# Optimization experiments

Measured on AMD Instinct MI355X. Metric: run time of the kernel, lower is better.

The kernel has to match this reference:

```python
import jax, jax.numpy as jnp
import numpy as np

B, T, D = 4, 2048, 1024
DEPTH = 4
LEAF_DIM = 256
NUM_LEAVES = 2 ** DEPTH          # 16
NUM_NODES = NUM_LEAVES - 1       # 15


def _uniform(key, shape, scale):
    s = 1.0 / np.sqrt(scale)
    return jax.random.uniform(key, shape, minval=-s, maxval=s, dtype=jnp.float32)


def setup_inputs() -> dict:
    key = jax.random.key(0)
    ks = jax.random.split(key, 8)
    x = jax.random.normal(ks[0], (B, T, D), dtype=jnp.float32)
    # gate params: Dense(1) per internal node, level-order layout
    node_w = _uniform(ks[1], (NUM_NODES, D), D)
    node_b = _uniform(ks[2], (NUM_NODES,), D)
    # leaf MLP params: D -> LEAF_DIM -> D, stacked over leaves
    w1 = _uniform(ks[3], (NUM_LEAVES, D, LEAF_DIM), D)
    b1 = _uniform(ks[4], (NUM_LEAVES, LEAF_DIM), D)
    w2 = _uniform(ks[5], (NUM_LEAVES, LEAF_DIM, D), LEAF_DIM)
    b2 = _uniform(ks[6], (NUM_LEAVES, D), LEAF_DIM)
    return {"x": x, "node_w": node_w, "node_b": node_b,
            "w1": w1, "b1": b1, "w2": w2, "b2": b2, "training": 0}


def _leaf_probs(x, node_w, node_b, depth):
    # gate activations for all internal nodes at once: [B,T,NUM_NODES]
    c = jax.nn.sigmoid(jnp.einsum('btd,nd->btn', x, node_w) + node_b)
    probs = jnp.ones(c.shape[:-1] + (1,), dtype=c.dtype)
    for m in range(depth):
        start = 2 ** m - 1
        cl = c[..., start:start + 2 ** m]          # gates at level m: [B,T,2^m]
        # left child gets c, right child gets (1-c); interleave preserves
        # the recursion's n -> (2n, 2n+1) indexing
        probs = jnp.stack([probs * cl, probs * (1.0 - cl)], axis=-1)
        probs = probs.reshape(probs.shape[:-2] + (-1,))
    return probs                                   # [B,T,NUM_LEAVES]


def reference(x, node_w, node_b, w1, b1, w2, b2, training):
    num_leaves = w1.shape[0]
    depth = int(np.log2(num_leaves))
    probs = _leaf_probs(x, node_w, node_b, depth)          # [B,T,L]
    # all leaf MLP hidden layers as one batched GEMM
    h = jax.nn.relu(jnp.einsum('btd,ldh->btlh', x, w1) + b1)
    # weight hidden by leaf probability, then contract l and h together so the
    # [B,T,L,D] per-leaf output is never materialized
    h = h * probs[..., None]
    out = jnp.einsum('btlh,lhd->btd', h, w2)
    out = out + jnp.einsum('btl,ld->btd', probs, b2)
    return out
```

## Files before the change

kernel.cpp:

```cpp
#include <hip/hip_runtime.h>
#include <stdint.h>

typedef unsigned short ushort_t;
typedef __bf16 bf16x8 __attribute__((ext_vector_type(8)));
typedef float f32x4 __attribute__((ext_vector_type(4)));

#define M_TOK 8192
#define K1 1024
#define N1 4096
#define K2 4160
#define N2 1024

template <int V> struct ic { static constexpr int value = V; };

__device__ __forceinline__ ushort_t f2bf(float f) {
  union { float f; unsigned u; } v; v.f = f;
  unsigned u = v.u;
  u += 0x7FFFu + ((u >> 16) & 1u);
  return (ushort_t)(u >> 16);
}

__device__ __forceinline__ void gload16(const void* g, void* l) {
  __builtin_amdgcn_global_load_lds((__attribute__((address_space(1))) void*)g,
                                   (__attribute__((address_space(3))) void*)l,
                                   16, 0, 0);
}

__global__ __launch_bounds__(256) void k_prep(
    const float* __restrict__ x, const float* __restrict__ node_w,
    const float* __restrict__ node_b, const float* __restrict__ w1,
    const float* __restrict__ w2, const float* __restrict__ b2,
    ushort_t* __restrict__ xb, float* __restrict__ probs,
    ushort_t* __restrict__ w1t, ushort_t* __restrict__ w2t,
    ushort_t* __restrict__ hp) {
  __shared__ ushort_t tile[64][68];
  const int b = blockIdx.x;
  if (b < 1024) {
    const int tr = threadIdx.x >> 4, tc = (threadIdx.x & 15) * 4;
    const int l = b >> 6, rem = b & 63;
    const int kt = rem >> 2, ht = rem & 3;
    const float* in = w1 + (size_t)l * K1 * 256;
#pragma unroll
    for (int rr = 0; rr < 4; ++rr) {
      int r = tr + rr * 16;
      float4 v = *(const float4*)(in + (size_t)(kt * 64 + r) * 256 + ht * 64 + tc);
      tile[r][tc+0] = f2bf(v.x); tile[r][tc+1] = f2bf(v.y);
      tile[r][tc+2] = f2bf(v.z); tile[r][tc+3] = f2bf(v.w);
    }
    __syncthreads();
#pragma unroll
    for (int rr = 0; rr < 4; ++rr) {
      int oh = tr + rr * 16;
      ushort4 o;
      o.x = tile[tc+0][oh]; o.y = tile[tc+1][oh];
      o.z = tile[tc+2][oh]; o.w = tile[tc+3][oh];
      *(ushort4*)(w1t + (size_t)(l * 256 + ht * 64 + oh) * K1 + kt * 64 + tc) = o;
    }
  } else if (b < 2048) {
    const int tr = threadIdx.x >> 4, tc = (threadIdx.x & 15) * 4;
    const int bb = b - 1024;
    const int l = bb >> 6, rem = bb & 63;
    const int ht = rem >> 4, dt = rem & 15;
    const float* in = w2 + (size_t)l * 256 * N2;
#pragma unroll
    for (int rr = 0; rr < 4; ++rr) {
      int r = tr + rr * 16;
      float4 v = *(const float4*)(in + (size_t)(ht * 64 + r) * N2 + dt * 64 + tc);
      tile[r][tc+0] = f2bf(v.x); tile[r][tc+1] = f2bf(v.y);
      tile[r][tc+2] = f2bf(v.z); tile[r][tc+3] = f2bf(v.w);
    }
    __syncthreads();
#pragma unroll
    for (int rr = 0; rr < 4; ++rr) {
      int od = tr + rr * 16;
      ushort4 o;
      o.x = tile[tc+0][od]; o.y = tile[tc+1][od];
      o.z = tile[tc+2][od]; o.w = tile[tc+3][od];
      *(ushort4*)(w2t + (size_t)(dt * 64 + od) * K2 + l * 256 + ht * 64 + tc) = o;
    }
  } else if (b < 2304) {
    int tid = (b - 2048) * 256 + threadIdx.x;
    int d = tid >> 6, cc = tid & 63;
    float v = (cc < 16) ? b2[cc * N2 + d] : 0.f;
    w2t[(size_t)d * K2 + 4096 + cc] = f2bf(v);
  } else {
    const int wid = threadIdx.x >> 6, lane = threadIdx.x & 63;
    const int t = (b - 2304) * 4 + wid;
    const float* xr = x + (size_t)t * K1;
    float xv[16];
#pragma unroll
    for (int j = 0; j < 4; ++j) {
      float4 v = *(const float4*)(xr + j * 256 + lane * 4);
      xv[4*j+0] = v.x; xv[4*j+1] = v.y; xv[4*j+2] = v.z; xv[4*j+3] = v.w;
    }
    ushort_t* xbr = xb + (size_t)t * K1;
#pragma unroll
    for (int j = 0; j < 4; ++j) {
      ushort4 o;
      o.x = f2bf(xv[4*j+0]); o.y = f2bf(xv[4*j+1]);
      o.z = f2bf(xv[4*j+2]); o.w = f2bf(xv[4*j+3]);
      *(ushort4*)(xbr + j * 256 + lane * 4) = o;
    }
    float c[15];
#pragma unroll
    for (int n = 0; n < 15; ++n) {
      float s = 0.f;
      const float* wr = node_w + n * K1;
#pragma unroll
      for (int j = 0; j < 4; ++j) {
        float4 w = *(const float4*)(wr + j * 256 + lane * 4);
        s += xv[4*j+0]*w.x + xv[4*j+1]*w.y + xv[4*j+2]*w.z + xv[4*j+3]*w.w;
      }
#pragma unroll
      for (int off = 32; off > 0; off >>= 1) s += __shfl_xor(s, off);
      float z = s + node_b[n];
      c[n] = 1.f / (1.f + __expf(-z));
    }
    if (lane < 16) {
      float p = 1.f;
#pragma unroll
      for (int m = 0; m < 4; ++m) {
        int jm = lane >> (4 - m);
        int node = (1 << m) - 1 + jm;
        int bit = (lane >> (3 - m)) & 1;
        p *= bit ? (1.f - c[node]) : c[node];
      }
      probs[t * 16 + lane] = p;
      hp[(size_t)t * K2 + 4096 + lane] = f2bf(p);
    }
    if (lane < 48) hp[(size_t)t * K2 + 4112 + lane] = 0;
  }
}

template <int NT, int LDA, int LDB, int MODE>
__global__ __launch_bounds__(512, 2) void k_gemm3(
    const ushort_t* __restrict__ A, const ushort_t* __restrict__ Bt,
    const float* __restrict__ probs, const float* __restrict__ b1,
    ushort_t* __restrict__ hp, float* __restrict__ out, int ntn) {
  constexpr int ATILE = 256 * 128;
  constexpr int BTILE = 128 * 128;
  constexpr int TBYTES = ATILE + BTILE;
  extern __shared__ char lds[];
  const int tid = threadIdx.x;
  int bid = blockIdx.x;
  const int nwg = gridDim.x;
  bid = (bid & 7) * (nwg >> 3) + (bid >> 3);
  const int bm = bid / ntn, bn = bid % ntn;

  const int wid = tid >> 6, lane = tid & 63;
  const int widM = wid >> 1, widN = wid & 1;
  const int lr = lane & 15, g = lane >> 4;

  const ushort_t* Ag = A + (size_t)bm * 256 * LDA;
  const ushort_t* Bg = Bt + (size_t)bn * 128 * LDB;

  auto stageHalf = [&](char* base, int kt, int part) {
#pragma unroll
    for (int r = 0; r < 2; ++r) {
      int s = tid + part * 1024 + r * 512;
      int row = s >> 3;
      int c16 = (s & 7) ^ (row & 7);
      gload16((const char*)(Ag + (size_t)row * LDA) + kt * 128 + (c16 << 4),
              base + s * 16);
    }
    {
      int s = tid + part * 512;
      int row = s >> 3;
      int c16 = (s & 7) ^ (row & 7);
      gload16((const char*)(Bg + (size_t)row * LDB) + kt * 128 + (c16 << 4),
              base + ATILE + s * 16);
    }
  };
  auto rdA = [&](char* base, int mi, int kk) -> bf16x8 {
    int row = widM * 64 + mi * 16 + lr;
    return *(const bf16x8*)(base + row * 128 + (((kk * 4 + g) ^ (lr & 7)) << 4));
  };
  auto rdB = [&](char* base, int nj, int kk) -> bf16x8 {
    int row = widN * 64 + nj * 16 + lr;
    return *(const bf16x8*)(base + ATILE + row * 128 + (((kk * 4 + g) ^ (lr & 7)) << 4));
  };

  f32x4 acc[4][4];
#pragma unroll
  for (int i = 0; i < 4; ++i)
#pragma unroll
    for (int j = 0; j < 4; ++j) acc[i][j] = (f32x4){0.f, 0.f, 0.f, 0.f};

  bf16x8 a01[2][4];
  bf16x8 bfr[2][8];
  bf16x8 a23[4];

  char* r0 = lds;
  char* r1 = lds + TBYTES;
  char* r2 = lds + 2 * TBYTES;

  stageHalf(r0, 0, 0); stageHalf(r0, 0, 1);
  stageHalf(r1, 1, 0); stageHalf(r1, 1, 1);
  asm volatile("s_waitcnt vmcnt(6)" ::: "memory");
  __builtin_amdgcn_sched_barrier(0);
  __builtin_amdgcn_s_barrier();
  __builtin_amdgcn_sched_barrier(0);
#pragma unroll
  for (int mi = 0; mi < 2; ++mi)
#pragma unroll
    for (int kk = 0; kk < 2; ++kk) a01[0][mi * 2 + kk] = rdA(r0, mi, kk);
#pragma unroll
  for (int nj = 0; nj < 4; ++nj)
#pragma unroll
    for (int kk = 0; kk < 2; ++kk) bfr[0][nj * 2 + kk] = rdB(r0, nj, kk);

  auto body = [&](auto PARC, int kt, char* cur, char* nxt, char* stg) {
    constexpr int P = decltype(PARC)::value;
#pragma unroll
    for (int mi = 0; mi < 2; ++mi)
#pragma unroll
      for (int kk = 0; kk < 2; ++kk) a23[mi * 2 + kk] = rdA(cur, mi + 2, kk);
    if (kt + 2 < NT) stageHalf(stg, kt + 2, 0);
    __builtin_amdgcn_sched_barrier(0);
    __builtin_amdgcn_s_setprio(1);
#pragma unroll
    for (int kk = 0; kk < 2; ++kk)
#pragma unroll
      for (int nj = 0; nj < 4; ++nj)
#pragma unroll
        for (int mi = 0; mi < 2; ++mi)
          acc[mi][nj] = __builtin_amdgcn_mfma_f32_16x16x32_bf16(
              a01[P][mi * 2 + kk], bfr[P][nj * 2 + kk], acc[mi][nj], 0, 0, 0);
    __builtin_amdgcn_s_setprio(0);
    if (kt + 1 < NT) {
      if (kt + 2 < NT) asm volatile("s_waitcnt vmcnt(3)" ::: "memory");
      else             asm volatile("s_waitcnt vmcnt(0)" ::: "memory");
      __builtin_amdgcn_sched_barrier(0);
      __builtin_amdgcn_s_barrier();
      __builtin_amdgcn_sched_barrier(0);
#pragma unroll
      for (int mi = 0; mi < 2; ++mi)
#pragma unroll
        for (int kk = 0; kk < 2; ++kk) a01[P ^ 1][mi * 2 + kk] = rdA(nxt, mi, kk);
#pragma unroll
      for (int nj = 0; nj < 4; ++nj)
#pragma unroll
        for (int kk = 0; kk < 2; ++kk) bfr[P ^ 1][nj * 2 + kk] = rdB(nxt, nj, kk);
      if (kt + 2 < NT) stageHalf(stg, kt + 2, 1);
    }
    __builtin_amdgcn_sched_barrier(0);
    __builtin_amdgcn_s_setprio(1);
#pragma unroll
    for (int kk = 0; kk < 2; ++kk)
#pragma unroll
      for (int nj = 0; nj < 4; ++nj)
#pragma unroll
        for (int mi = 0; mi < 2; ++mi)
          acc[2 + mi][nj] = __builtin_amdgcn_mfma_f32_16x16x32_bf16(
              a23[mi * 2 + kk], bfr[P][nj * 2 + kk], acc[2 + mi][nj], 0, 0, 0);
    __builtin_amdgcn_s_setprio(0);
  };

  int kt = 0;
#pragma unroll 1
  for (int it = 0; it < NT / 2; ++it) {
    body(ic<0>{}, kt, r0, r1, r2); ++kt;
    { char* t = r0; r0 = r1; r1 = r2; r2 = t; }
    body(ic<1>{}, kt, r0, r1, r2); ++kt;
    { char* t = r0; r0 = r1; r1 = r2; r2 = t; }
  }
  if constexpr (NT & 1) body(ic<0>{}, kt, r0, r1, r2);

  const int rowb = bm * 256 + widM * 64 + g * 4;
  const int colb = bn * 128 + widN * 64 + lr;
  if (MODE == 0) {
    const int leaf = bn >> 1;
#pragma unroll
    for (int mi = 0; mi < 4; ++mi) {
      int rbase = rowb + mi * 16;
      float pm[4];
#pragma unroll
      for (int rg = 0; rg < 4; ++rg)
        pm[rg] = probs[(size_t)(rbase + rg) * 16 + leaf];
#pragma unroll
      for (int nj = 0; nj < 4; ++nj) {
        float bias = b1[colb + nj * 16];
#pragma unroll
        for (int rg = 0; rg < 4; ++rg) {
          float v = acc[mi][nj][rg] + bias;
          v = v > 0.f ? v : 0.f;
          v *= pm[rg];
          hp[(size_t)(rbase + rg) * K2 + colb + nj * 16] = f2bf(v);
        }
      }
    }
  } else {
#pragma unroll
    for (int mi = 0; mi < 4; ++mi) {
      int rbase = rowb + mi * 16;
#pragma unroll
      for (int nj = 0; nj < 4; ++nj)
#pragma unroll
        for (int rg = 0; rg < 4; ++rg)
          out[(size_t)(rbase + rg) * N2 + colb + nj * 16] = acc[mi][nj][rg];
    }
  }
}

extern "C" void kernel_launch(void* const* d_in, const int* in_sizes, int n_in,
                              void* d_out, int out_size, void* d_ws, size_t ws_size,
                              hipStream_t stream) {
  const float* x      = (const float*)d_in[0];
  const float* node_w = (const float*)d_in[1];
  const float* node_b = (const float*)d_in[2];
  const float* w1     = (const float*)d_in[3];
  const float* b1     = (const float*)d_in[4];
  const float* w2     = (const float*)d_in[5];
  const float* b2     = (const float*)d_in[6];
  float* out = (float*)d_out;

  char* ws = (char*)d_ws;
  ushort_t* xb    = (ushort_t*)(ws);
  ushort_t* w1t   = (ushort_t*)(ws + 16777216);
  ushort_t* w2t   = (ushort_t*)(ws + 25165824);
  ushort_t* hp    = (ushort_t*)(ws + 33685504);
  float*    probs = (float*)   (ws + 101842944);

  k_prep<<<4352, 256, 0, stream>>>(x, node_w, node_b, w1, w2, b2,
                                   xb, probs, w1t, w2t, hp);
  k_gemm3<16, K1, K1, 0><<<1024, 512, 147456, stream>>>(
      xb, w1t, probs, b1, hp, nullptr, N1 / 128);
  k_gemm3<65, K2, K2, 1><<<256, 512, 147456, stream>>>(
      hp, w2t, nullptr, nullptr, nullptr, out, N2 / 128);
}
```

Before: 182.8 us.

## Replace 512-thread triple-buffered GEMM with 256-thread double-buffered larger per-wave tiles

The GEMM kernel goes from 8 waves with a 3-stage LDS pipeline and interleaved half-stage loads to 4 waves, each computing 128 rows, with a simple double-buffered loop. The first GEMM uses a 256x256 tile so each block covers exactly one leaf, and the second uses 256x128. The aim is more register-level reuse per wave and fewer LDS reads per MFMA. In exchange it loses the finer prefetch interleaving and priority hints, waits on vmcnt(0) and a barrier every k-step, and drops to one block per CU with much higher register pressure.

```diff
diff --git a/kernel.cpp b/kernel.cpp
--- a/kernel.cpp
+++ b/kernel.cpp
@@ -132,14 +132,18 @@
   }
 }
 
-template <int NT, int LDA, int LDB, int MODE>
-__global__ __launch_bounds__(512, 2) void k_gemm3(
+template <int NT, int LDA, int LDB, int BN, int MODE>
+__global__ __launch_bounds__(256, 1) void k_gemm4(
     const ushort_t* __restrict__ A, const ushort_t* __restrict__ Bt,
     const float* __restrict__ probs, const float* __restrict__ b1,
     ushort_t* __restrict__ hp, float* __restrict__ out, int ntn) {
+  constexpr int FN = BN / 32;
   constexpr int ATILE = 256 * 128;
-  constexpr int BTILE = 128 * 128;
-  constexpr int TBYTES = ATILE + BTILE;
+  constexpr int BTILE = BN * 128;
+  constexpr int TB = ATILE + BTILE;
+  constexpr int SA = ATILE / (256 * 16);
+  constexpr int SB = BTILE / (256 * 16);
+
   extern __shared__ char lds[];
   const int tid = threadIdx.x;
   int bid = blockIdx.x;
@@ -152,19 +156,20 @@
   const int lr = lane & 15, g = lane >> 4;
 
   const ushort_t* Ag = A + (size_t)bm * 256 * LDA;
-  const ushort_t* Bg = Bt + (size_t)bn * 128 * LDB;
-
-  auto stageHalf = [&](char* base, int kt, int part) {
-#pragma unroll
-    for (int r = 0; r < 2; ++r) {
-      int s = tid + part * 1024 + r * 512;
+  const ushort_t* Bg = Bt + (size_t)bn * BN * LDB;
+
+  auto stage = [&](char* base, int kt) {
+#pragma unroll
+    for (int r = 0; r < SA; ++r) {
+      int s = tid + r * 256;
       int row = s >> 3;
       int c16 = (s & 7) ^ (row & 7);
       gload16((const char*)(Ag + (size_t)row * LDA) + kt * 128 + (c16 << 4),
               base + s * 16);
     }
-    {
-      int s = tid + part * 512;
+#pragma unroll
+    for (int r = 0; r < SB; ++r) {
+      int s = tid + r * 256;
       int row = s >> 3;
       int c16 = (s & 7) ^ (row & 7);
       gload16((const char*)(Bg + (size_t)row * LDB) + kt * 128 + (c16 << 4),
@@ -172,113 +177,75 @@
     }
   };
   auto rdA = [&](char* base, int mi, int kk) -> bf16x8 {
-    int row = widM * 64 + mi * 16 + lr;
+    int row = widM * 128 + mi * 16 + lr;
     return *(const bf16x8*)(base + row * 128 + (((kk * 4 + g) ^ (lr & 7)) << 4));
   };
   auto rdB = [&](char* base, int nj, int kk) -> bf16x8 {
-    int row = widN * 64 + nj * 16 + lr;
+    int row = widN * (BN / 2) + nj * 16 + lr;
     return *(const bf16x8*)(base + ATILE + row * 128 + (((kk * 4 + g) ^ (lr & 7)) << 4));
   };
 
-  f32x4 acc[4][4];
-#pragma unroll
-  for (int i = 0; i < 4; ++i)
-#pragma unroll
-    for (int j = 0; j < 4; ++j) acc[i][j] = (f32x4){0.f, 0.f, 0.f, 0.f};
-
-  bf16x8 a01[2][4];
-  bf16x8 bfr[2][8];
-  bf16x8 a23[4];
-
-  char* r0 = lds;
-  char* r1 = lds + TBYTES;
-  char* r2 = lds + 2 * TBYTES;
-
-  stageHalf(r0, 0, 0); stageHalf(r0, 0, 1);
-  stageHalf(r1, 1, 0); stageHalf(r1, 1, 1);
-  asm volatile("s_waitcnt vmcnt(6)" ::: "memory");
+  f32x4 acc[8][FN];
+#pragma unroll
+  for (int i = 0; i < 8; ++i)
+#pragma unroll
+    for (int j = 0; j < FN; ++j) acc[i][j] = (f32x4){0.f, 0.f, 0.f, 0.f};
+
+  stage(lds, 0);
+  asm volatile("s_waitcnt vmcnt(0)" ::: "memory");
   __builtin_amdgcn_sched_barrier(0);
   __builtin_amdgcn_s_barrier();
   __builtin_amdgcn_sched_barrier(0);
-#pragma unroll
-  for (int mi = 0; mi < 2; ++mi)
-#pragma unroll
-    for (int kk = 0; kk < 2; ++kk) a01[0][mi * 2 + kk] = rdA(r0, mi, kk);
-#pragma unroll
-  for (int nj = 0; nj < 4; ++nj)
-#pragma unroll
-    for (int kk = 0; kk < 2; ++kk) bfr[0][nj * 2 + kk] = rdB(r0, nj, kk);
-
-  auto body = [&](auto PARC, int kt, char* cur, char* nxt, char* stg) {
-    constexpr int P = decltype(PARC)::value;
-#pragma unroll
-    for (int mi = 0; mi < 2; ++mi)
-#pragma unroll
-      for (int kk = 0; kk < 2; ++kk) a23[mi * 2 + kk] = rdA(cur, mi + 2, kk);
-    if (kt + 2 < NT) stageHalf(stg, kt + 2, 0);
+
+  auto body = [&](auto CURC, int kt) {
+    constexpr int cur = decltype(CURC)::value;
+    char* buf = lds + cur * TB;
+    char* nbuf = lds + (cur ^ 1) * TB;
+    if (kt + 1 < NT) stage(nbuf, kt + 1);
     __builtin_amdgcn_sched_barrier(0);
-    __builtin_amdgcn_s_setprio(1);
+    bf16x8 a[8][2], b[FN][2];
+#pragma unroll
+    for (int kk = 0; kk < 2; ++kk) {
+#pragma unroll
+      for (int mi = 0; mi < 8; ++mi) a[mi][kk] = rdA(buf, mi, kk);
+#pragma unroll
+      for (int nj = 0; nj < FN; ++nj) b[nj][kk] = rdB(buf, nj, kk);
+    }
 #pragma unroll
     for (int kk = 0; kk < 2; ++kk)
 #pragma unroll
-      for (int nj = 0; nj < 4; ++nj)
-#pragma unroll
-        for (int mi = 0; mi < 2; ++mi)
+      for (int nj = 0; nj < FN; ++nj)
+#pragma unroll
+        for (int mi = 0; mi < 8; ++mi)
           acc[mi][nj] = __builtin_amdgcn_mfma_f32_16x16x32_bf16(
-              a01[P][mi * 2 + kk], bfr[P][nj * 2 + kk], acc[mi][nj], 0, 0, 0);
-    __builtin_amdgcn_s_setprio(0);
-    if (kt + 1 < NT) {
-      if (kt + 2 < NT) asm volatile("s_waitcnt vmcnt(3)" ::: "memory");
-      else             asm volatile("s_waitcnt vmcnt(0)" ::: "memory");
-      __builtin_amdgcn_sched_barrier(0);
-      __builtin_amdgcn_s_barrier();
-      __builtin_amdgcn_sched_barrier(0);
-#pragma unroll
-      for (int mi = 0; mi < 2; ++mi)
-#pragma unroll
-        for (int kk = 0; kk < 2; ++kk) a01[P ^ 1][mi * 2 + kk] = rdA(nxt, mi, kk);
-#pragma unroll
-      for (int nj = 0; nj < 4; ++nj)
-#pragma unroll
-        for (int kk = 0; kk < 2; ++kk) bfr[P ^ 1][nj * 2 + kk] = rdB(nxt, nj, kk);
-      if (kt + 2 < NT) stageHalf(stg, kt + 2, 1);
-    }
+              a[mi][kk], b[nj][kk], acc[mi][nj], 0, 0, 0);
+    asm volatile("s_waitcnt vmcnt(0)" ::: "memory");
     __builtin_amdgcn_sched_barrier(0);
-    __builtin_amdgcn_s_setprio(1);
-#pragma unroll
-    for (int kk = 0; kk < 2; ++kk)
-#pragma unroll
-      for (int nj = 0; nj < 4; ++nj)
-#pragma unroll
-        for (int mi = 0; mi < 2; ++mi)
-          acc[2 + mi][nj] = __builtin_amdgcn_mfma_f32_16x16x32_bf16(
-              a23[mi * 2 + kk], bfr[P][nj * 2 + kk], acc[2 + mi][nj], 0, 0, 0);
-    __builtin_amdgcn_s_setprio(0);
+    __builtin_amdgcn_s_barrier();
+    __builtin_amdgcn_sched_barrier(0);
   };
 
   int kt = 0;
 #pragma unroll 1
   for (int it = 0; it < NT / 2; ++it) {
-    body(ic<0>{}, kt, r0, r1, r2); ++kt;
-    { char* t = r0; r0 = r1; r1 = r2; r2 = t; }
-    body(ic<1>{}, kt, r0, r1, r2); ++kt;
-    { char* t = r0; r0 = r1; r1 = r2; r2 = t; }
+    body(ic<0>{}, kt); ++kt;
+    body(ic<1>{}, kt); ++kt;
   }
-  if constexpr (NT & 1) body(ic<0>{}, kt, r0, r1, r2);
-
-  const int rowb = bm * 256 + widM * 64 + g * 4;
-  const int colb = bn * 128 + widN * 64 + lr;
+  if constexpr (NT & 1) body(ic<0>{}, kt);
+
+  const int rowb = bm * 256 + widM * 128 + g * 4;
+  const int colb = bn * BN + widN * (BN / 2) + lr;
   if (MODE == 0) {
-    const int leaf = bn >> 1;
-#pragma unroll
-    for (int mi = 0; mi < 4; ++mi) {
+    const int leaf = bn;
+#pragma unroll
+    for (int mi = 0; mi < 8; ++mi) {
       int rbase = rowb + mi * 16;
       float pm[4];
 #pragma unroll
       for (int rg = 0; rg < 4; ++rg)
         pm[rg] = probs[(size_t)(rbase + rg) * 16 + leaf];
 #pragma unroll
-      for (int nj = 0; nj < 4; ++nj) {
+      for (int nj = 0; nj < FN; ++nj) {
         float bias = b1[colb + nj * 16];
 #pragma unroll
         for (int rg = 0; rg < 4; ++rg) {
@@ -291,10 +258,10 @@
     }
   } else {
 #pragma unroll
-    for (int mi = 0; mi < 4; ++mi) {
+    for (int mi = 0; mi < 8; ++mi) {
       int rbase = rowb + mi * 16;
 #pragma unroll
-      for (int nj = 0; nj < 4; ++nj)
+      for (int nj = 0; nj < FN; ++nj)
 #pragma unroll
         for (int rg = 0; rg < 4; ++rg)
           out[(size_t)(rbase + rg) * N2 + colb + nj * 16] = acc[mi][nj][rg];
@@ -323,8 +290,8 @@
 
   k_prep<<<4352, 256, 0, stream>>>(x, node_w, node_b, w1, w2, b2,
                                    xb, probs, w1t, w2t, hp);
-  k_gemm3<16, K1, K1, 0><<<1024, 512, 147456, stream>>>(
-      xb, w1t, probs, b1, hp, nullptr, N1 / 128);
-  k_gemm3<65, K2, K2, 1><<<256, 512, 147456, stream>>>(
+  k_gemm4<16, K1, K1, 256, 0><<<512, 256, 131072, stream>>>(
+      xb, w1t, probs, b1, hp, nullptr, N1 / 256);
+  k_gemm4<65, K2, K2, 128, 1><<<256, 256, 98304, stream>>>(
       hp, w2t, nullptr, nullptr, nullptr, out, N2 / 128);
 }
```

New measurement: 322.8 us. 76.5% more time.
